# Optimization experiments

Measured on AMD Instinct MI355X. Metric: run time of the kernel, lower is better.

## Reference

```python
import jax, jax.numpy as jnp
import numpy as np

STRIDE = 16
H = 100
W = 100
C = 1024
A = 9  # anchors per location
IOU_THRESH = 0.7
MIN_SIZE = 16.0


def _conv2d(x, w, b):
    # x: [N,C,H,W], w: [O,I,kh,kw] (torch OIHW), 'same' padding, stride 1
    y = jax.lax.conv_general_dilated(
        x, w, window_strides=(1, 1), padding='SAME',
        dimension_numbers=('NCHW', 'OIHW', 'NCHW'))
    return y + b[None, :, None, None]


def _nms_keep(boxes, valid, iou_thresh):
    # boxes: [N,4] (y1,x1,y2,x2) sorted by descending score; valid: [N] bool
    n = boxes.shape[0]
    y1, x1, y2, x2 = boxes[:, 0], boxes[:, 1], boxes[:, 2], boxes[:, 3]
    areas = (y2 - y1) * (x2 - x1)
    idx = jnp.arange(n)

    def body(i, keep):
        iy1 = jnp.maximum(y1[i], y1)
        ix1 = jnp.maximum(x1[i], x1)
        iy2 = jnp.minimum(y2[i], y2)
        ix2 = jnp.minimum(x2[i], x2)
        inter = jnp.maximum(iy2 - iy1, 0.0) * jnp.maximum(ix2 - ix1, 0.0)
        iou = inter / (areas[i] + areas - inter + 1e-8)
        suppress = (iou > iou_thresh) & (idx > i)
        return jnp.where(keep[i], keep & ~suppress, keep)

    return jax.lax.fori_loop(0, n, body, valid)


def _make_anchor_map():
    ratios = np.array([0.5, 1.0, 2.0])
    sizes = np.array([128.0, 256.0, 512.0])
    ah = (sizes[:, None] * np.sqrt(ratios)[None, :]).reshape(-1)  # [9]
    aw = (sizes[:, None] / np.sqrt(ratios)[None, :]).reshape(-1)  # [9]
    cy = (np.arange(H) + 0.5) * STRIDE
    cx = (np.arange(W) + 0.5) * STRIDE
    am = np.zeros((H, W, A, 4), dtype=np.float32)
    am[..., 0] = cy[:, None, None]
    am[..., 1] = cx[None, :, None]
    am[..., 2] = ah[None, None, :]
    am[..., 3] = aw[None, None, :]
    return jnp.asarray(am.reshape(H, W, A * 4))


def setup_inputs() -> dict:
    key = jax.random.key(0)
    ks = jax.random.split(key, 4)
    feature_map = jax.random.normal(ks[0], (1, C, H, W), jnp.float32)
    # module init: normal(0, 0.01) weights, zero biases
    w1 = jax.random.normal(ks[1], (C, C, 3, 3), jnp.float32) * 0.01
    b1 = jnp.zeros((C,), jnp.float32)
    w_cls = jax.random.normal(ks[2], (A, C, 1, 1), jnp.float32) * 0.01
    b_cls = jnp.zeros((A,), jnp.float32)
    w_box = jax.random.normal(ks[3], (A * 4, C, 1, 1), jnp.float32) * 0.01
    b_box = jnp.zeros((A * 4,), jnp.float32)
    return {
        'feature_map': feature_map,
        'image_shape': jnp.array([3, H * STRIDE, W * STRIDE], jnp.int32),
        'anchor_map': _make_anchor_map(),
        'anchor_valid_map': jnp.ones((H, W, A), jnp.int32),
        'max_proposals_pre_nms': 6000,
        'max_proposals_post_nms': 300,
        'w1': w1, 'b1': b1,
        'w_cls': w_cls, 'b_cls': b_cls,
        'w_box': w_box, 'b_box': b_box,
    }


def reference(feature_map, image_shape, anchor_map, anchor_valid_map,
              max_proposals_pre_nms, max_proposals_post_nms,
              w1, b1, w_cls, b_cls, w_box, b_box):
    pre = int(max_proposals_pre_nms)
    post = int(max_proposals_post_nms)

    y = jax.nn.relu(_conv2d(feature_map, w1, b1))
    objectness_score_map = jax.nn.sigmoid(_conv2d(y, w_cls, b_cls))  # [1,9,H,W]
    box_deltas_map = _conv2d(y, w_box, b_box)                        # [1,36,H,W]
    # NCHW -> NHWC, like permute(0,2,3,1)
    objectness_score_map = jnp.transpose(objectness_score_map, (0, 2, 3, 1))
    box_deltas_map = jnp.transpose(box_deltas_map, (0, 2, 3, 1))

    h, w, a = anchor_valid_map.shape
    n = h * w * a
    anchors = anchor_map.reshape(n, 4)                # (cy, cx, ah, aw)
    scores = objectness_score_map.reshape(n)
    deltas = jax.lax.stop_gradient(box_deltas_map.reshape(n, 4))  # .detach()
    # allow_edge_proposals=True -> no valid filtering

    # decode (means=0, stds=1): center = c + t*s, size = s*exp(t)
    center = anchors[:, 0:2] + deltas[:, 0:2] * anchors[:, 2:4]
    size = anchors[:, 2:4] * jnp.exp(deltas[:, 2:4])
    proposals = jnp.concatenate([center - 0.5 * size, center + 0.5 * size], axis=1)

    # argsort ascending then flip == descending (matches torch code)
    order = jnp.argsort(scores)[::-1][:pre]
    proposals = proposals[order]
    scores_sorted = scores[order]

    # clip to image
    y1x1 = jnp.maximum(proposals[:, 0:2], 0.0)
    y2 = jnp.minimum(proposals[:, 2], image_shape[1].astype(proposals.dtype))
    x2 = jnp.minimum(proposals[:, 3], image_shape[2].astype(proposals.dtype))
    proposals = jnp.concatenate([y1x1, y2[:, None], x2[:, None]], axis=1)

    height = proposals[:, 2] - proposals[:, 0]
    width = proposals[:, 3] - proposals[:, 1]
    valid = (height >= MIN_SIZE) & (width >= MIN_SIZE)

    keep = _nms_keep(proposals, valid, IOU_THRESH)

    # fixed-shape selection of first `post` kept boxes (score-ordered)
    pos = jnp.where(keep, jnp.arange(pre), pre)
    pos = jnp.sort(pos)[:post]
    ok = pos < pre
    safe = jnp.minimum(pos, pre - 1)
    out_proposals = jnp.where(ok[:, None], proposals[safe], 0.0)  # [post,4]

    return objectness_score_map, box_deltas_map, out_proposals
```

## Files before the change

### kernel.cpp

```cpp
#include <hip/hip_runtime.h>
#include <hip/hip_fp16.h>
#include <stdint.h>

#define HH 100
#define WW 100
#define NPIX 10000
#define CIN 1024
#define COUT 1024
#define NA 9
#define NANCH 90000
#define PRE 6000
#define POST 300
#define SORTN 131072
#define MASKW 96
#define NW 94
#define K9 9216
#define SPAD 10404
#define WSCALE 1024.0f
#define KH 48

typedef unsigned short u16;
typedef _Float16 f16x8 __attribute__((ext_vector_type(8)));
typedef float f32x4 __attribute__((ext_vector_type(4)));

__global__ __launch_bounds__(256) void xsplit(
    const float* __restrict__ x, u16* __restrict__ xt1, u16* __restrict__ xt2)
{
    __shared__ unsigned sh[32][257];
    const int t = threadIdx.x;
    const int px0 = blockIdx.x * 32;
    const int ci0 = blockIdx.y * 256;
    for (int it = 0; it < 32; ++it) {
        int idx = it * 256 + t;
        int a = idx >> 5, b = idx & 31;
        int p = px0 + b;
        float v = (p < NPIX) ? x[(size_t)(ci0 + a) * NPIX + p] : 0.f;
        __half h1 = __float2half_rn(v);
        __half h2 = __float2half_rn(v - __half2float(h1));
        sh[b][a] = ((unsigned)__half_as_ushort(h1) << 16) | __half_as_ushort(h2);
    }
    __syncthreads();
    for (int it = 0; it < 8; ++it) {
        int u = it * 256 + t;
        int pl = u >> 6, cq = u & 63;
        int p = px0 + pl;
        if (p >= NPIX) continue;
        int r = p / 100, c = p - r * 100;
        int spx = (r + 1) * 102 + (c + 1);
        unsigned w0 = sh[pl][cq * 4 + 0], w1 = sh[pl][cq * 4 + 1];
        unsigned w2 = sh[pl][cq * 4 + 2], w3 = sh[pl][cq * 4 + 3];
        ushort4 v1 = make_ushort4((u16)(w0 >> 16), (u16)(w1 >> 16), (u16)(w2 >> 16), (u16)(w3 >> 16));
        ushort4 v2 = make_ushort4((u16)(w0 & 0xffff), (u16)(w1 & 0xffff), (u16)(w2 & 0xffff), (u16)(w3 & 0xffff));
        size_t o = (size_t)spx * 1024 + ci0 + cq * 4;
        *(ushort4*)&xt1[o] = v1;
        *(ushort4*)&xt2[o] = v2;
    }
}

__global__ __launch_bounds__(256) void xborder(u16* __restrict__ xt1, u16* __restrict__ xt2)
{
    const int idx = blockIdx.x;
    int spx;
    if (idx < 102) spx = idx;
    else if (idx < 204) spx = 10302 + (idx - 102);
    else { int k = idx - 204; spx = (1 + (k >> 1)) * 102 + (k & 1) * 101; }
    const int t = threadIdx.x;
    size_t o = (size_t)spx * 1024 + t * 4;
    *(ushort4*)&xt1[o] = make_ushort4(0, 0, 0, 0);
    *(ushort4*)&xt2[o] = make_ushort4(0, 0, 0, 0);
}

__global__ __launch_bounds__(256) void wsplit(
    const float* __restrict__ w1, u16* __restrict__ wp1, u16* __restrict__ wp2)
{
    __shared__ float sw[K9];
    const int t = threadIdx.x;
    const int co = blockIdx.x;
    for (int it = 0; it < 36; ++it)
        sw[it * 256 + t] = w1[(size_t)co * K9 + it * 256 + t];
    __syncthreads();
    for (int tap = 0; tap < 9; ++tap) {
        for (int it = 0; it < 4; ++it) {
            int ci = it * 256 + t;
            float v = sw[ci * 9 + tap] * WSCALE;
            __half h1 = __float2half_rn(v);
            __half h2 = __float2half_rn(v - __half2float(h1));
            size_t o = (size_t)tap * (COUT * 1024) + (size_t)co * 1024 + ci;
            wp1[o] = __half_as_ushort(h1);
            wp2[o] = __half_as_ushort(h2);
        }
    }
}

__global__ __launch_bounds__(256, 3) void conv_mfma(
    const u16* __restrict__ xt1, const u16* __restrict__ xt2,
    const u16* __restrict__ wp1, const u16* __restrict__ wp2,
    const float* __restrict__ b1, float* __restrict__ y)
{
    __shared__ __align__(16) char lds[40960];
    const int t = threadIdx.x;
    const int co0 = blockIdx.x * 128;
    const int px0 = blockIdx.y * 128;
    const int wave = t >> 6, lane = t & 63;
    const int wm = (wave >> 1) * 64;
    const int wn = (wave & 1) * 64;

    int gA[2], gB[2], lA[2], lB[2];
#pragma unroll
    for (int q = 0; q < 2; ++q) {
        int u = t + q * 256;
        int row = u >> 2, ch = u & 3;
        gA[q] = (co0 + row) * 1024 + ch * 8;
        int p = px0 + row; if (p > NPIX - 1) p = NPIX - 1;
        int r = p / 100, c = p - r * 100;
        gB[q] = ((r + 1) * 102 + c + 1) * 1024 + ch * 8;
        lA[q] = row * 80 + ch * 16;
        lB[q] = 20480 + row * 80 + ch * 16;
    }
    const int fA = (wm + (lane & 15)) * 80 + (lane >> 4) * 16;
    const int fB = 20480 + (wn + (lane & 15)) * 80 + (lane >> 4) * 16;

    f32x4 acc[4][4] = {};

    for (int tap = 0; tap < 9; ++tap) {
        const int dy = tap / 3;
        const int toff = ((dy - 1) * 102 + (tap - dy * 3) - 1) * 1024;
        const int wtap = tap << 20;
        for (int ci0 = 0; ci0 < 1024; ci0 += 32) {
            __syncthreads();
#pragma unroll
            for (int q = 0; q < 2; ++q) {
                uint4 a1 = *(const uint4*)(wp1 + (gA[q] + wtap + ci0));
                uint4 a2 = *(const uint4*)(wp2 + (gA[q] + wtap + ci0));
                uint4 b1v = *(const uint4*)(xt1 + (gB[q] + toff + ci0));
                uint4 b2v = *(const uint4*)(xt2 + (gB[q] + toff + ci0));
                *(uint4*)(lds + lA[q])         = a1;
                *(uint4*)(lds + lA[q] + 10240) = a2;
                *(uint4*)(lds + lB[q])         = b1v;
                *(uint4*)(lds + lB[q] + 10240) = b2v;
            }
            __syncthreads();
            f16x8 A1[4], A2[4], B1[4], B2[4];
#pragma unroll
            for (int mi = 0; mi < 4; ++mi) {
                A1[mi] = *(const f16x8*)(lds + fA + mi * 1280);
                A2[mi] = *(const f16x8*)(lds + fA + mi * 1280 + 10240);
            }
#pragma unroll
            for (int ni = 0; ni < 4; ++ni) {
                B1[ni] = *(const f16x8*)(lds + fB + ni * 1280);
                B2[ni] = *(const f16x8*)(lds + fB + ni * 1280 + 10240);
            }
#pragma unroll
            for (int mi = 0; mi < 4; ++mi)
#pragma unroll
                for (int ni = 0; ni < 4; ++ni) {
                    acc[mi][ni] = __builtin_amdgcn_mfma_f32_16x16x32_f16(A1[mi], B1[ni], acc[mi][ni], 0, 0, 0);
                    acc[mi][ni] = __builtin_amdgcn_mfma_f32_16x16x32_f16(A1[mi], B2[ni], acc[mi][ni], 0, 0, 0);
                    acc[mi][ni] = __builtin_amdgcn_mfma_f32_16x16x32_f16(A2[mi], B1[ni], acc[mi][ni], 0, 0, 0);
                }
        }
    }

    const int q4 = (lane >> 4) * 4, nl = lane & 15;
    const float inv = 1.0f / WSCALE;
#pragma unroll
    for (int mi = 0; mi < 4; ++mi) {
        const int cob = co0 + wm + mi * 16 + q4;
        const float bb0 = b1[cob + 0], bb1 = b1[cob + 1];
        const float bb2 = b1[cob + 2], bb3 = b1[cob + 3];
#pragma unroll
        for (int ni = 0; ni < 4; ++ni) {
            const int px = px0 + wn + ni * 16 + nl;
            if (px < NPIX) {
                y[(size_t)(cob + 0) * NPIX + px] = fmaxf(acc[mi][ni][0] * inv + bb0, 0.f);
                y[(size_t)(cob + 1) * NPIX + px] = fmaxf(acc[mi][ni][1] * inv + bb1, 0.f);
                y[(size_t)(cob + 2) * NPIX + px] = fmaxf(acc[mi][ni][2] * inv + bb2, 0.f);
                y[(size_t)(cob + 3) * NPIX + px] = fmaxf(acc[mi][ni][3] * inv + bb3, 0.f);
            }
        }
    }
}

__global__ __launch_bounds__(256) void wh_prep(
    const float* __restrict__ wcls, const float* __restrict__ wbox,
    float* __restrict__ wh)
{
    int e = blockIdx.x * 256 + threadIdx.x;
    if (e >= CIN * KH) return;
    int c = e / KH, k = e - c * KH;
    float v = 0.f;
    if (k < 9) v = wcls[k * CIN + c];
    else if (k < 45) v = wbox[(k - 9) * CIN + c];
    wh[e] = v;
}

__global__ __launch_bounds__(256) void rpn_head(
    const float* __restrict__ y, const float* __restrict__ wh,
    const float* __restrict__ bcls, const float* __restrict__ bbox,
    const float* __restrict__ am, const int* __restrict__ ishape,
    float* __restrict__ out_scores, float* __restrict__ out_deltas,
    float4* __restrict__ boxes, unsigned long long* __restrict__ keys)
{
    __shared__ float red[4][64][KH + 1];
    const int t = threadIdx.x;
    const int lane = t & 63;
    const int q = __builtin_amdgcn_readfirstlane(t >> 6);
    const int p = blockIdx.x * 64 + lane;
    const int pp = (p < NPIX) ? p : (NPIX - 1);

    float acc[45];
#pragma unroll
    for (int k = 0; k < 45; ++k) acc[k] = 0.f;

    const float* __restrict__ yq  = y  + (size_t)q * 256 * NPIX + pp;
    const float* __restrict__ whq = wh + (size_t)q * 256 * KH;
    for (int c = 0; c < 256; ++c) {
        float yv = yq[(size_t)c * NPIX];
        const float* wr = whq + c * KH;
#pragma unroll
        for (int k = 0; k < 45; ++k) acc[k] += yv * wr[k];
    }

#pragma unroll
    for (int k = 0; k < 45; ++k) red[q][lane][k] = acc[k];
    __syncthreads();

    if (t >= 64 || p >= NPIX) return;

    float s[45];
#pragma unroll
    for (int k = 0; k < 45; ++k)
        s[k] = (red[0][lane][k] + red[1][lane][k]) + (red[2][lane][k] + red[3][lane][k]);

    const float imh = (float)ishape[1], imw = (float)ishape[2];
#pragma unroll
    for (int a = 0; a < 9; ++a) {
        const int i = p * NA + a;
        float logit = s[a] + bcls[a];
        float score = 1.f / (1.f + expf(-logit));
        float d0 = s[9 + a * 4 + 0] + bbox[a * 4 + 0];
        float d1 = s[9 + a * 4 + 1] + bbox[a * 4 + 1];
        float d2 = s[9 + a * 4 + 2] + bbox[a * 4 + 2];
        float d3 = s[9 + a * 4 + 3] + bbox[a * 4 + 3];
        out_scores[i] = score;
        out_deltas[i * 4 + 0] = d0;
        out_deltas[i * 4 + 1] = d1;
        out_deltas[i * 4 + 2] = d2;
        out_deltas[i * 4 + 3] = d3;

        float cy = am[i * 4 + 0], cx = am[i * 4 + 1];
        float ah = am[i * 4 + 2], aw = am[i * 4 + 3];
        float ctry = cy + d0 * ah, ctrx = cx + d1 * aw;
        float hh = ah * expf(d2), ww = aw * expf(d3);
        float y1 = fmaxf(ctry - 0.5f * hh, 0.f);
        float x1 = fmaxf(ctrx - 0.5f * ww, 0.f);
        float y2 = fminf(ctry + 0.5f * hh, imh);
        float x2 = fminf(ctrx + 0.5f * ww, imw);
        boxes[i] = make_float4(y1, x1, y2, x2);
        unsigned sb = __float_as_uint(score);
        keys[i] = ((unsigned long long)sb << 32) | (unsigned)i;
    }
}

__global__ __launch_bounds__(256) void key_pad(unsigned long long* __restrict__ keys)
{
    int i = NANCH + blockIdx.x * 256 + threadIdx.x;
    if (i < SORTN) keys[i] = 0ull;
}

__global__ __launch_bounds__(256) void bitonic_local(unsigned long long* keys)
{
    __shared__ unsigned long long s[2048];
    const int base = blockIdx.x * 2048, t = threadIdx.x;
    for (int k = t; k < 2048; k += 256) s[k] = keys[base + k];
    for (int L = 2; L <= 2048; L <<= 1) {
        for (int d = L >> 1; d >= 1; d >>= 1) {
            __syncthreads();
            for (int pr = t; pr < 1024; pr += 256) {
                int i = ((pr & ~(d - 1)) << 1) | (pr & (d - 1));
                int j = i + d;
                bool desc = (((base + i) & L) == 0);
                unsigned long long va = s[i], vb = s[j];
                bool sw = desc ? (va < vb) : (va > vb);
                if (sw) { s[i] = vb; s[j] = va; }
            }
        }
    }
    __syncthreads();
    for (int k = t; k < 2048; k += 256) keys[base + k] = s[k];
}

__global__ __launch_bounds__(256) void bitonic_gpass(unsigned long long* keys, int L, int d)
{
    int pr = blockIdx.x * 256 + threadIdx.x;
    int i = ((pr & ~(d - 1)) << 1) | (pr & (d - 1));
    int j = i + d;
    bool desc = ((i & L) == 0);
    unsigned long long va = keys[i], vb = keys[j];
    bool sw = desc ? (va < vb) : (va > vb);
    if (sw) { keys[i] = vb; keys[j] = va; }
}

__global__ __launch_bounds__(256) void bitonic_lmerge(unsigned long long* keys, int L)
{
    __shared__ unsigned long long s[2048];
    const int base = blockIdx.x * 2048, t = threadIdx.x;
    for (int k = t; k < 2048; k += 256) s[k] = keys[base + k];
    const bool desc = ((base & L) == 0);
    for (int d = 1024; d >= 1; d >>= 1) {
        __syncthreads();
        for (int pr = t; pr < 1024; pr += 256) {
            int i = ((pr & ~(d - 1)) << 1) | (pr & (d - 1));
            int j = i + d;
            unsigned long long va = s[i], vb = s[j];
            bool sw = desc ? (va < vb) : (va > vb);
            if (sw) { s[i] = vb; s[j] = va; }
        }
    }
    __syncthreads();
    for (int k = t; k < 2048; k += 256) keys[base + k] = s[k];
}

__global__ __launch_bounds__(256) void gather_sorted(
    const unsigned long long* __restrict__ keys, const float4* __restrict__ boxes,
    float4* __restrict__ box_s, unsigned long long* __restrict__ validw)
{
    int s = blockIdx.x * 256 + threadIdx.x;
    bool valid = false;
    if (s < PRE) {
        unsigned idx = (unsigned)(keys[s] & 0xffffffffull);
        float4 b = boxes[idx];
        box_s[s] = b;
        valid = ((b.z - b.x) >= 16.f) && ((b.w - b.y) >= 16.f);
    }
    unsigned long long bal = __ballot(valid);
    if ((threadIdx.x & 63) == 0) validw[s >> 6] = bal;
}

__global__ __launch_bounds__(128) void nms_mask(
    const float4* __restrict__ box_s, unsigned long long* __restrict__ mask)
{
    const int i = blockIdx.x;
    const int w = threadIdx.x;
    if (w >= NW) return;
    float4 bi = box_s[i];
    float areai = (bi.z - bi.x) * (bi.w - bi.y);
    unsigned long long m = 0ull;
    const int j0 = w * 64;
    if (j0 + 63 > i) {
#pragma unroll 4
        for (int b = 0; b < 64; ++b) {
            int j = j0 + b;
            if (j <= i || j >= PRE) continue;
            float4 bj = box_s[j];
            float areaj = (bj.z - bj.x) * (bj.w - bj.y);
            float iy1 = fmaxf(bi.x, bj.x), ix1 = fmaxf(bi.y, bj.y);
            float iy2 = fminf(bi.z, bj.z), ix2 = fminf(bi.w, bj.w);
            float inter = fmaxf(iy2 - iy1, 0.f) * fmaxf(ix2 - ix1, 0.f);
            float iou = inter / (areai + areaj - inter + 1e-8f);
            if (iou > 0.7f) m |= (1ull << b);
        }
    }
    mask[(size_t)i * MASKW + w] = m;
}

__global__ __launch_bounds__(64) void nms_scan(
    const unsigned long long* __restrict__ mask,
    const unsigned long long* __restrict__ validw,
    unsigned long long* __restrict__ keepw)
{
    const int l = threadIdx.x;
    unsigned long long r0 = ~validw[l];
    unsigned long long r1 = (l < NW - 64) ? ~validw[64 + l] : ~0ull;

    unsigned long long p0[16], p1[16];
#pragma unroll
    for (int k = 0; k < 16; ++k) {
        p0[k] = mask[(size_t)k * MASKW + l];
        p1[k] = (l < NW - 64) ? mask[(size_t)k * MASKW + 64 + l] : 0ull;
    }
    int kept = 0;
    for (int w = 0; w < NW && kept < POST; ++w) {
        unsigned long long Wc = (w < 64) ? __shfl(r0, w) : __shfl(r1, w - 64);
#pragma unroll 16
        for (int b = 0; b < 64; ++b) {
            int i = w * 64 + b;
            if (i >= PRE) break;
            int slot = i & 15;
            unsigned long long m0 = p0[slot], m1 = p1[slot];
            int nxt = i + 16;
            if (nxt < PRE) {
                p0[slot] = mask[(size_t)nxt * MASKW + l];
                p1[slot] = (l < NW - 64) ? mask[(size_t)nxt * MASKW + 64 + l] : 0ull;
            }
            if (!((Wc >> b) & 1ull)) {
                r0 |= m0; r1 |= m1;
                Wc = (w < 64) ? __shfl(r0, w) : __shfl(r1, w - 64);
                ++kept;
            }
        }
    }
    keepw[l] = ~r0;
    if (l < NW - 64) keepw[64 + l] = ~r1;
}

__global__ __launch_bounds__(256) void out_gather(
    const unsigned long long* __restrict__ keepw,
    const float4* __restrict__ box_s, float* __restrict__ outp)
{
    __shared__ unsigned long long kw_s[NW];
    __shared__ int prefix[NW];
    const int t = threadIdx.x;
    if (t < NW) kw_s[t] = keepw[t];
    __syncthreads();
    if (t == 0) {
        int cum = 0;
        for (int w = 0; w < NW; ++w) { prefix[w] = cum; cum += __popcll(kw_s[w]); }
    }
    for (int k = t; k < POST * 4; k += 256) outp[k] = 0.f;
    __syncthreads();
    for (int i = t; i < PRE; i += 256) {
        int w = i >> 6, b = i & 63;
        unsigned long long kw = kw_s[w];
        if ((kw >> b) & 1ull) {
            int rank = prefix[w] + __popcll(kw & ((1ull << b) - 1ull));
            if (rank < POST) {
                float4 bx = box_s[i];
                outp[rank * 4 + 0] = bx.x;
                outp[rank * 4 + 1] = bx.y;
                outp[rank * 4 + 2] = bx.z;
                outp[rank * 4 + 3] = bx.w;
            }
        }
    }
}

extern "C" void kernel_launch(void* const* d_in, const int* in_sizes, int n_in,
                              void* d_out, int out_size, void* d_ws, size_t ws_size,
                              hipStream_t stream)
{
    const float* x      = (const float*)d_in[0];
    const int*   ishape = (const int*)  d_in[1];
    const float* am     = (const float*)d_in[2];
    const float* w1   = (const float*)d_in[6];
    const float* b1   = (const float*)d_in[7];
    const float* wcls = (const float*)d_in[8];
    const float* bcls = (const float*)d_in[9];
    const float* wbox = (const float*)d_in[10];
    const float* bbox = (const float*)d_in[11];
    float* out = (float*)d_out;

    char* ws = (char*)d_ws;
    size_t off = 0;
    float* y  = (float*)(ws + off);  off += (size_t)COUT * NPIX * 4;
    u16* xt1  = (u16*)(ws + off);    off += (size_t)SPAD * 1024 * 2;
    u16* xt2  = (u16*)(ws + off);    off += (size_t)SPAD * 1024 * 2;
    u16* wp1  = (u16*)(ws + off);    off += (size_t)9 * COUT * 1024 * 2;
    u16* wp2  = (u16*)(ws + off);    off += (size_t)9 * COUT * 1024 * 2;
    float4* boxes = (float4*)(ws + off);              off += (size_t)NANCH * 16;
    unsigned long long* keys = (unsigned long long*)(ws + off); off += (size_t)SORTN * 8;
    float4* box_s = (float4*)(ws + off);              off += (size_t)PRE * 16;
    unsigned long long* validw = (unsigned long long*)(ws + off); off += 96 * 8;
    unsigned long long* keepw  = (unsigned long long*)(ws + off); off += 96 * 8;
    unsigned long long* maskb  = (unsigned long long*)(ws + off); off += (size_t)PRE * MASKW * 8;
    float* wh = (float*)(ws + off);  off += (size_t)CIN * KH * 4;

    xsplit<<<dim3(313, 4), 256, 0, stream>>>(x, xt1, xt2);
    xborder<<<404, 256, 0, stream>>>(xt1, xt2);
    wsplit<<<COUT, 256, 0, stream>>>(w1, wp1, wp2);
    wh_prep<<<(CIN * KH + 255) / 256, 256, 0, stream>>>(wcls, wbox, wh);
    conv_mfma<<<dim3(8, 79), 256, 0, stream>>>(xt1, xt2, wp1, wp2, b1, y);
    rpn_head<<<(NPIX + 63) / 64, 256, 0, stream>>>(y, wh, bcls, bbox, am, ishape,
                                                   out, out + NANCH, boxes, keys);
    key_pad<<<(SORTN - NANCH + 255) / 256, 256, 0, stream>>>(keys);
    bitonic_local<<<SORTN / 2048, 256, 0, stream>>>(keys);
    for (int L = 4096; L <= SORTN; L <<= 1) {
        for (int d = L >> 1; d >= 2048; d >>= 1)
            bitonic_gpass<<<SORTN / 512, 256, 0, stream>>>(keys, L, d);
        bitonic_lmerge<<<SORTN / 2048, 256, 0, stream>>>(keys, L);
    }
    gather_sorted<<<24, 256, 0, stream>>>(keys, boxes, box_s, validw);
    nms_mask<<<PRE, 128, 0, stream>>>(box_s, maskb);
    nms_scan<<<1, 64, 0, stream>>>(maskb, validw, keepw);
    out_gather<<<1, 256, 0, stream>>>(keepw, box_s, out + (size_t)NANCH * 5);
}
```

Measured before the change: 1.288 ms.

## Double-buffer conv GEMM with direct global-to-LDS loads and wider pixel tile

Measured after the change: 1.138 ms. -11.6%, faster.

```diff
diff --git a/kernel.cpp b/kernel.cpp
--- a/kernel.cpp
+++ b/kernel.cpp
@@ -19,9 +19,20 @@
 #define WSCALE 1024.0f
 #define KH 48
 
+#define PXT 160
+#define ABYTES 8192
+#define BBYTES 10240
+#define BUFB 36864
+#define NSTEP 288
+
 typedef unsigned short u16;
 typedef _Float16 f16x8 __attribute__((ext_vector_type(8)));
 typedef float f32x4 __attribute__((ext_vector_type(4)));
+
+__device__ __forceinline__ void gload16(const u16* g, char* l)
+{
+    __builtin_amdgcn_global_load_lds((const void*)g, (void*)l, 16, 0, 0);
+}
 
 __global__ __launch_bounds__(256) void xsplit(
     const float* __restrict__ x, u16* __restrict__ xt1, u16* __restrict__ xt2)
@@ -92,75 +103,97 @@
     }
 }
 
-__global__ __launch_bounds__(256, 3) void conv_mfma(
+__global__ __launch_bounds__(256, 2) void conv_mfma(
     const u16* __restrict__ xt1, const u16* __restrict__ xt2,
     const u16* __restrict__ wp1, const u16* __restrict__ wp2,
     const float* __restrict__ b1, float* __restrict__ y)
 {
-    __shared__ __align__(16) char lds[40960];
+    __shared__ __align__(16) char lds[2 * BUFB];
     const int t = threadIdx.x;
     const int co0 = blockIdx.x * 128;
-    const int px0 = blockIdx.y * 128;
-    const int wave = t >> 6, lane = t & 63;
-    const int wm = (wave >> 1) * 64;
-    const int wn = (wave & 1) * 64;
-
-    int gA[2], gB[2], lA[2], lB[2];
-#pragma unroll
-    for (int q = 0; q < 2; ++q) {
-        int u = t + q * 256;
-        int row = u >> 2, ch = u & 3;
-        gA[q] = (co0 + row) * 1024 + ch * 8;
-        int p = px0 + row; if (p > NPIX - 1) p = NPIX - 1;
-        int r = p / 100, c = p - r * 100;
-        gB[q] = ((r + 1) * 102 + c + 1) * 1024 + ch * 8;
-        lA[q] = row * 80 + ch * 16;
-        lB[q] = 20480 + row * 80 + ch * 16;
-    }
-    const int fA = (wm + (lane & 15)) * 80 + (lane >> 4) * 16;
-    const int fB = 20480 + (wn + (lane & 15)) * 80 + (lane >> 4) * 16;
-
-    f32x4 acc[4][4] = {};
-
-    for (int tap = 0; tap < 9; ++tap) {
-        const int dy = tap / 3;
-        const int toff = ((dy - 1) * 102 + (tap - dy * 3) - 1) * 1024;
-        const int wtap = tap << 20;
-        for (int ci0 = 0; ci0 < 1024; ci0 += 32) {
-            __syncthreads();
-#pragma unroll
-            for (int q = 0; q < 2; ++q) {
-                uint4 a1 = *(const uint4*)(wp1 + (gA[q] + wtap + ci0));
-                uint4 a2 = *(const uint4*)(wp2 + (gA[q] + wtap + ci0));
-                uint4 b1v = *(const uint4*)(xt1 + (gB[q] + toff + ci0));
-                uint4 b2v = *(const uint4*)(xt2 + (gB[q] + toff + ci0));
-                *(uint4*)(lds + lA[q])         = a1;
-                *(uint4*)(lds + lA[q] + 10240) = a2;
-                *(uint4*)(lds + lB[q])         = b1v;
-                *(uint4*)(lds + lB[q] + 10240) = b2v;
-            }
-            __syncthreads();
-            f16x8 A1[4], A2[4], B1[4], B2[4];
-#pragma unroll
-            for (int mi = 0; mi < 4; ++mi) {
-                A1[mi] = *(const f16x8*)(lds + fA + mi * 1280);
-                A2[mi] = *(const f16x8*)(lds + fA + mi * 1280 + 10240);
-            }
-#pragma unroll
-            for (int ni = 0; ni < 4; ++ni) {
-                B1[ni] = *(const f16x8*)(lds + fB + ni * 1280);
-                B2[ni] = *(const f16x8*)(lds + fB + ni * 1280 + 10240);
-            }
-#pragma unroll
-            for (int mi = 0; mi < 4; ++mi)
-#pragma unroll
-                for (int ni = 0; ni < 4; ++ni) {
-                    acc[mi][ni] = __builtin_amdgcn_mfma_f32_16x16x32_f16(A1[mi], B1[ni], acc[mi][ni], 0, 0, 0);
-                    acc[mi][ni] = __builtin_amdgcn_mfma_f32_16x16x32_f16(A1[mi], B2[ni], acc[mi][ni], 0, 0, 0);
-                    acc[mi][ni] = __builtin_amdgcn_mfma_f32_16x16x32_f16(A2[mi], B1[ni], acc[mi][ni], 0, 0, 0);
-                }
-        }
-    }
+    const int px0 = blockIdx.y * PXT;
+    const int lane = t & 63;
+    const int wv = __builtin_amdgcn_readfirstlane(t >> 6);
+    const int wm = (wv >> 1) * 64;
+    const int wn = (wv & 1) * 80;
+
+    const int qs = (lane & 3) ^ ((lane >> 3) & 3);
+    const int aln = (lane >> 2) * 1024 + qs * 8;
+
+    const int ar0 = wv * 32, ar1 = wv * 32 + 16;
+    const size_t aOff0 = (size_t)(co0 + ar0) * 1024 + aln;
+    const size_t aOff1 = (size_t)(co0 + ar1) * 1024 + aln;
+
+    const int nb = (wv < 2) ? 3 : 2;
+    size_t bOff[3]; int bLds[3];
+#pragma unroll
+    for (int s = 0; s < 3; ++s) {
+        int r0 = (wv + 4 * s) * 16;
+        if (r0 >= PXT) r0 = 0;
+        int p = px0 + r0 + (lane >> 2);
+        if (p > NPIX - 1) p = NPIX - 1;
+        int rr = p / 100, cc = p - rr * 100;
+        bOff[s] = (size_t)((rr + 1) * 102 + cc + 1) * 1024 + qs * 8;
+        bLds[s] = r0 * 64;
+    }
+
+    const int qf = ((lane >> 4) ^ (((lane & 15) >> 1) & 3)) * 16;
+    const int fA = (wm + (lane & 15)) * 64 + qf;
+    const int fB = 16384 + (wn + (lane & 15)) * 64 + qf;
+
+    f32x4 acc[4][5] = {};
+
+    auto STAGE = [&](int buf, int tap, int ci0) {
+        const int dy = (tap * 11) >> 5;
+        const int tsh = (dy - 1) * 102 + (tap - dy * 3) - 1;
+        const size_t adelta = (size_t)tap * 1048576 + ci0;
+        const ptrdiff_t bdelta = (ptrdiff_t)tsh * 1024 + ci0;
+        char* lb = lds + buf * BUFB;
+        gload16(wp1 + aOff0 + adelta, lb + ar0 * 64);
+        gload16(wp1 + aOff1 + adelta, lb + ar1 * 64);
+        gload16(wp2 + aOff0 + adelta, lb + ABYTES + ar0 * 64);
+        gload16(wp2 + aOff1 + adelta, lb + ABYTES + ar1 * 64);
+#pragma unroll
+        for (int s = 0; s < 3; ++s) {
+            if (s < nb) {
+                gload16(xt1 + (ptrdiff_t)bOff[s] + bdelta, lb + 16384 + bLds[s]);
+                gload16(xt2 + (ptrdiff_t)bOff[s] + bdelta, lb + 26624 + bLds[s]);
+            }
+        }
+    };
+
+    auto COMPUTE = [&](int buf) {
+        const char* lb = lds + buf * BUFB;
+        f16x8 A1[4], A2[4], B1[5], B2[5];
+#pragma unroll
+        for (int mi = 0; mi < 4; ++mi) {
+            A1[mi] = *(const f16x8*)(lb + fA + mi * 1024);
+            A2[mi] = *(const f16x8*)(lb + ABYTES + fA + mi * 1024);
+        }
+#pragma unroll
+        for (int ni = 0; ni < 5; ++ni) {
+            B1[ni] = *(const f16x8*)(lb + fB + ni * 1024);
+            B2[ni] = *(const f16x8*)(lb + BBYTES + fB + ni * 1024);
+        }
+#pragma unroll
+        for (int mi = 0; mi < 4; ++mi)
+#pragma unroll
+            for (int ni = 0; ni < 5; ++ni) {
+                acc[mi][ni] = __builtin_amdgcn_mfma_f32_16x16x32_f16(A1[mi], B1[ni], acc[mi][ni], 0, 0, 0);
+                acc[mi][ni] = __builtin_amdgcn_mfma_f32_16x16x32_f16(A1[mi], B2[ni], acc[mi][ni], 0, 0, 0);
+                acc[mi][ni] = __builtin_amdgcn_mfma_f32_16x16x32_f16(A2[mi], B1[ni], acc[mi][ni], 0, 0, 0);
+            }
+    };
+
+    STAGE(0, 0, 0);
+    __syncthreads();
+    for (int kk = 0; kk < NSTEP - 1; ++kk) {
+        const int kn = kk + 1;
+        STAGE(kn & 1, kn >> 5, (kn & 31) << 5);
+        COMPUTE(kk & 1);
+        __syncthreads();
+    }
+    COMPUTE((NSTEP - 1) & 1);
 
     const int q4 = (lane >> 4) * 4, nl = lane & 15;
     const float inv = 1.0f / WSCALE;
@@ -170,7 +203,7 @@
         const float bb0 = b1[cob + 0], bb1 = b1[cob + 1];
         const float bb2 = b1[cob + 2], bb3 = b1[cob + 3];
 #pragma unroll
-        for (int ni = 0; ni < 4; ++ni) {
+        for (int ni = 0; ni < 5; ++ni) {
             const int px = px0 + wn + ni * 16 + nl;
             if (px < NPIX) {
                 y[(size_t)(cob + 0) * NPIX + px] = fmaxf(acc[mi][ni][0] * inv + bb0, 0.f);
@@ -470,7 +503,7 @@
     xborder<<<404, 256, 0, stream>>>(xt1, xt2);
     wsplit<<<COUT, 256, 0, stream>>>(w1, wp1, wp2);
     wh_prep<<<(CIN * KH + 255) / 256, 256, 0, stream>>>(wcls, wbox, wh);
-    conv_mfma<<<dim3(8, 79), 256, 0, stream>>>(xt1, xt2, wp1, wp2, b1, y);
+    conv_mfma<<<dim3(8, (NPIX + PXT - 1) / PXT), 256, 0, stream>>>(xt1, xt2, wp1, wp2, b1, y);
     rpn_head<<<(NPIX + 63) / 64, 256, 0, stream>>>(y, wh, bcls, bbox, am, ishape,
                                                    out, out + NANCH, boxes, keys);
     key_pad<<<(SORTN - NANCH + 255) / 256, 256, 0, stream>>>(keys);
```
